# Kernel optimization log

Measured on AMD Instinct MI355X. Metric: run time of the kernel, lower is better.

The kernel has to match this reference:

```python
import jax, jax.numpy as jnp
import numpy as np

B, S, DIM = 1, 2048, 4096
NH, NKV, HD = 32, 8, 128
REPEATS = NH // NKV
ROPE_THETA = 10000.0


def setup_inputs() -> dict:
    key = jax.random.key(0)
    ks = jax.random.split(key, 6)
    x = jax.random.normal(ks[0], (B, S, DIM), jnp.float32) * 0.02
    wq = jax.random.normal(ks[1], (NH * HD, DIM), jnp.float32) * 0.02
    wk = jax.random.normal(ks[2], (NKV * HD, DIM), jnp.float32) * 0.02
    wv = jax.random.normal(ks[3], (NKV * HD, DIM), jnp.float32) * 0.02
    wo = jax.random.normal(ks[4], (DIM, NH * HD), jnp.float32) * 0.02
    # rotary frequencies (real cos/sin form of complex freqs_cis)
    inv_freq = 1.0 / (ROPE_THETA ** (jnp.arange(0, HD, 2, dtype=jnp.float32) / HD))
    ang = jnp.arange(S, dtype=jnp.float32)[:, None] * inv_freq[None, :]  # [S, HD//2]
    freqs_cos = jnp.cos(ang)
    freqs_sin = jnp.sin(ang)
    positions = jnp.arange(S, dtype=jnp.int32)  # prompt phase: all positions
    # additive causal mask
    mask = jnp.where(jnp.tril(jnp.ones((S, S), bool)), 0.0, -1e9).astype(jnp.float32)
    cache_k = jnp.zeros((B, S, NKV, HD), jnp.float32)
    cache_v = jnp.zeros((B, S, NKV, HD), jnp.float32)
    return dict(x=x, wq=wq, wk=wk, wv=wv, wo=wo, freqs_cos=freqs_cos,
                freqs_sin=freqs_sin, cache_k=cache_k, cache_v=cache_v,
                positions=positions, mask=mask)


def apply_rope(t, cos, sin):
    # t: [b, s, h, d]; pairs are (d0,d1),(d2,d3),... matching view_as_complex
    tr = t[..., 0::2]
    ti = t[..., 1::2]
    c = cos[None, :, None, :]
    s = sin[None, :, None, :]
    out_r = tr * c - ti * s
    out_i = tr * s + ti * c
    return jnp.stack([out_r, out_i], axis=-1).reshape(t.shape)


def reference(x, wq, wk, wv, wo, freqs_cos, freqs_sin, cache_k, cache_v, positions, mask):
    b, s, _ = x.shape
    xq = jnp.einsum('bsd,od->bso', x, wq).reshape(b, s, NH, HD)
    xk = jnp.einsum('bsd,od->bso', x, wk).reshape(b, s, NKV, HD)
    xv = jnp.einsum('bsd,od->bso', x, wv).reshape(b, s, NKV, HD)
    xq = apply_rope(xq, freqs_cos, freqs_sin)
    xk = apply_rope(xk, freqs_cos, freqs_sin)
    # KV-cache scatter (prompt phase writes; output uses fresh xk/xv here)
    cache_k = cache_k.at[:, positions].set(xk)
    cache_v = cache_v.at[:, positions].set(xv)
    # GQA: repeat_interleave kv heads to match query heads
    k = jnp.repeat(xk, REPEATS, axis=2).transpose(0, 2, 1, 3)  # [b, NH, s, HD]
    v = jnp.repeat(xv, REPEATS, axis=2).transpose(0, 2, 1, 3)
    q = xq.transpose(0, 2, 1, 3)
    scale = HD ** -0.5
    scores = jnp.einsum('bhqd,bhkd->bhqk', q, k) * scale + mask[None, None]
    probs = jax.nn.softmax(scores.astype(jnp.float32), axis=-1).astype(q.dtype)
    out = jnp.einsum('bhqk,bhkd->bhqd', probs, v)
    out = out.transpose(0, 2, 1, 3).reshape(b, s, NH * HD)
    return jnp.einsum('bso,do->bsd', out, wo)
```

## Files before the change

### kernel.cpp

```cpp
#include <hip/hip_runtime.h>
#include <hip/hip_bf16.h>
#include <stdint.h>

typedef __bf16 bf16_t;
typedef __attribute__((ext_vector_type(8))) __bf16 bf16x8;
typedef __attribute__((ext_vector_type(4))) float f32x4;
typedef __attribute__((ext_vector_type(8))) unsigned short u16x8;

#define S_LEN 2048
#define DIM   4096
#define QKVN  6144
#define NHEAD 32
#define HDIM  128

typedef __attribute__((address_space(1))) unsigned int as1_u32;
typedef __attribute__((address_space(3))) unsigned int as3_u32;

__device__ __forceinline__ unsigned short f2bf(float f) {
  unsigned u = __builtin_bit_cast(unsigned, f);
  u += 0x7fffu + ((u >> 16) & 1u);
  return (unsigned short)(u >> 16);
}

__device__ __forceinline__ void gload_lds16(const void* g, void* l) {
  __builtin_amdgcn_global_load_lds(
      (as1_u32*)(unsigned long long)(uintptr_t)g,
      (as3_u32*)(unsigned int)(uintptr_t)l,
      16, 0, 0);
}

__global__ __launch_bounds__(256) void cvt5_kernel(const float* __restrict__ x,
                                                   const float* __restrict__ wq,
                                                   const float* __restrict__ wk,
                                                   const float* __restrict__ wv,
                                                   const float* __restrict__ wo,
                                                   ushort4* __restrict__ xb,
                                                   ushort4* __restrict__ wqkvb,
                                                   ushort4* __restrict__ wob) {
  const long N0 = 2097152;
  const long N1 = N0 + 4194304;
  const long N2 = N1 + 1048576;
  const long N3 = N2 + 1048576;
  const long N4 = N3 + 4194304;
  long idx = (long)blockIdx.x * 256 + threadIdx.x;
  long stride = (long)gridDim.x * 256;
  for (long i = idx; i < N4; i += stride) {
    const float4* s; ushort4* d; long o;
    if (i < N0)      { s = (const float4*)x;  d = xb;              o = i; }
    else if (i < N1) { s = (const float4*)wq; d = wqkvb;           o = i - N0; }
    else if (i < N2) { s = (const float4*)wk; d = wqkvb + 4194304; o = i - N1; }
    else if (i < N3) { s = (const float4*)wv; d = wqkvb + 5242880; o = i - N2; }
    else             { s = (const float4*)wo; d = wob;             o = i - N3; }
    float4 v = s[o];
    ushort4 r;
    r.x = f2bf(v.x); r.y = f2bf(v.y); r.z = f2bf(v.z); r.w = f2bf(v.w);
    d[o] = r;
  }
}

__device__ __forceinline__ bf16x8 fld(const char* half, int row, int chunk) {
  return *(const bf16x8*)(half + row * 128 + ((chunk ^ (row & 7)) << 4));
}

template <int OUTF32>
__global__ __launch_bounds__(512, 2) void gemm8q(const bf16_t* __restrict__ A,
                                                 const bf16_t* __restrict__ B,
                                                 void* __restrict__ Cout,
                                                 int M, int N, int K, int nxt) {
  __shared__ char lds[114688];
  const int tid = threadIdx.x;
  const int lane = tid & 63, w = tid >> 6;
  const int wm = w >> 2, wn = w & 3;
  const int lg = lane >> 4, lr = lane & 15;
  const int nwg = gridDim.x;
  const int orig = blockIdx.x;
  const int wgid = (orig & 7) * (nwg >> 3) + (orig >> 3);
  const int bx = wgid % nxt, by = wgid / nxt;
  const long rowA = (long)by * 256;
  const long rowB = (long)bx * 192;

  f32x4 acc[8][3];
  const f32x4 z4 = {0.f, 0.f, 0.f, 0.f};
#pragma unroll
  for (int i = 0; i < 8; ++i)
#pragma unroll
    for (int j = 0; j < 3; ++j) acc[i][j] = z4;

  const int r0 = tid >> 3, sl = tid & 7;
  const long xo  = (long)((sl ^ (r0 & 7)) << 3);
  const long aof = (rowA + r0) * (long)K + xo;
  const long bof = (rowB + r0) * (long)K + xo;
  const long j1  = (long)64 * K;
  const long h1  = (long)128 * K;
  const int ld0 = tid * 16, ld1 = (tid + 512) * 16, ld2 = (tid + 1024) * 16;

#define QSTG_A(K0, HALF, DBUF)                                                 \
  { char* hp = lds + (DBUF) * 57344 + (HALF) * 16384;                          \
    gload_lds16(A + aof + (HALF) * h1 + (K0),      hp + ld0);                  \
    gload_lds16(A + aof + (HALF) * h1 + j1 + (K0), hp + ld1); }
#define QSTG_B(K0, DBUF)                                                       \
  { char* bp = lds + (DBUF) * 57344 + 32768;                                   \
    gload_lds16(B + bof + (K0),          bp + ld0);                            \
    gload_lds16(B + bof + j1 + (K0),     bp + ld1);                            \
    gload_lds16(B + bof + 2 * j1 + (K0), bp + ld2); }

  const int nt = K >> 6;
  const int brow = wn * 48;

  QSTG_A(0, 0, 0); QSTG_A(0, 1, 0); QSTG_B(0, 0);
  QSTG_B(64, 1);
  asm volatile("s_waitcnt vmcnt(3)" ::: "memory");
  __builtin_amdgcn_s_barrier();

  bf16x8 af[8][2], bf_[3][2];

  for (int t = 0; t < nt; ++t) {
    const int d = t & 1;
    const char* Ah = lds + d * 57344 + wm * 16384;
    const char* Br = lds + d * 57344 + 32768;
    const int k1 = (t + 1) << 6, k2 = (t + 2) << 6;
#pragma unroll
    for (int m = 0; m < 2; ++m) {
      af[m][0] = fld(Ah, m * 16 + lr, lg);
      af[m][1] = fld(Ah, m * 16 + lr, 4 + lg);
    }
#pragma unroll
    for (int n = 0; n < 3; ++n) {
      bf_[n][0] = fld(Br, brow + n * 16 + lr, lg);
      bf_[n][1] = fld(Br, brow + n * 16 + lr, 4 + lg);
    }
    if (t + 1 < nt) QSTG_A(k1, 0, d ^ 1);
    __builtin_amdgcn_s_barrier();
    asm volatile("s_waitcnt lgkmcnt(0)" ::: "memory");
    __builtin_amdgcn_sched_barrier(0);
    __builtin_amdgcn_s_setprio(1);
#pragma unroll
    for (int m = 0; m < 2; ++m)
#pragma unroll
      for (int n = 0; n < 3; ++n) {
        acc[m][n] = __builtin_amdgcn_mfma_f32_16x16x32_bf16(af[m][0], bf_[n][0], acc[m][n], 0, 0, 0);
        acc[m][n] = __builtin_amdgcn_mfma_f32_16x16x32_bf16(af[m][1], bf_[n][1], acc[m][n], 0, 0, 0);
      }
    __builtin_amdgcn_s_setprio(0);
    __builtin_amdgcn_s_barrier();
#pragma unroll
    for (int m = 2; m < 4; ++m) {
      af[m][0] = fld(Ah, m * 16 + lr, lg);
      af[m][1] = fld(Ah, m * 16 + lr, 4 + lg);
    }
    if (t + 1 < nt) QSTG_A(k1, 1, d ^ 1);
    __builtin_amdgcn_s_barrier();
    asm volatile("s_waitcnt lgkmcnt(0)" ::: "memory");
    __builtin_amdgcn_sched_barrier(0);
    __builtin_amdgcn_s_setprio(1);
#pragma unroll
    for (int m = 2; m < 4; ++m)
#pragma unroll
      for (int n = 0; n < 3; ++n) {
        acc[m][n] = __builtin_amdgcn_mfma_f32_16x16x32_bf16(af[m][0], bf_[n][0], acc[m][n], 0, 0, 0);
        acc[m][n] = __builtin_amdgcn_mfma_f32_16x16x32_bf16(af[m][1], bf_[n][1], acc[m][n], 0, 0, 0);
      }
    __builtin_amdgcn_s_setprio(0);
    __builtin_amdgcn_s_barrier();
#pragma unroll
    for (int m = 4; m < 6; ++m) {
      af[m][0] = fld(Ah, m * 16 + lr, lg);
      af[m][1] = fld(Ah, m * 16 + lr, 4 + lg);
    }
    if (t + 2 < nt) QSTG_B(k2, d);
    __builtin_amdgcn_s_barrier();
    asm volatile("s_waitcnt lgkmcnt(0)" ::: "memory");
    __builtin_amdgcn_sched_barrier(0);
    __builtin_amdgcn_s_setprio(1);
#pragma unroll
    for (int m = 4; m < 6; ++m)
#pragma unroll
      for (int n = 0; n < 3; ++n) {
        acc[m][n] = __builtin_amdgcn_mfma_f32_16x16x32_bf16(af[m][0], bf_[n][0], acc[m][n], 0, 0, 0);
        acc[m][n] = __builtin_amdgcn_mfma_f32_16x16x32_bf16(af[m][1], bf_[n][1], acc[m][n], 0, 0, 0);
      }
    __builtin_amdgcn_s_setprio(0);
    __builtin_amdgcn_s_barrier();
#pragma unroll
    for (int m = 6; m < 8; ++m) {
      af[m][0] = fld(Ah, m * 16 + lr, lg);
      af[m][1] = fld(Ah, m * 16 + lr, 4 + lg);
    }
    __builtin_amdgcn_s_barrier();
    asm volatile("s_waitcnt lgkmcnt(0)" ::: "memory");
    __builtin_amdgcn_sched_barrier(0);
    __builtin_amdgcn_s_setprio(1);
#pragma unroll
    for (int m = 6; m < 8; ++m)
#pragma unroll
      for (int n = 0; n < 3; ++n) {
        acc[m][n] = __builtin_amdgcn_mfma_f32_16x16x32_bf16(af[m][0], bf_[n][0], acc[m][n], 0, 0, 0);
        acc[m][n] = __builtin_amdgcn_mfma_f32_16x16x32_bf16(af[m][1], bf_[n][1], acc[m][n], 0, 0, 0);
      }
    __builtin_amdgcn_s_setprio(0);
    if (t + 2 < nt) {
      asm volatile("s_waitcnt vmcnt(3)" ::: "memory");
    } else {
      asm volatile("s_waitcnt vmcnt(0)" ::: "memory");
    }
    __builtin_amdgcn_s_barrier();
  }
#undef QSTG_A
#undef QSTG_B

  const long crow = rowA + wm * 128;
  const long ccol = rowB + wn * 48;
  if (OUTF32) {
    float* C = (float*)Cout;
#pragma unroll
    for (int mf = 0; mf < 8; ++mf)
#pragma unroll
      for (int j = 0; j < 4; ++j) {
        long row = crow + mf * 16 + lg * 4 + j;
        float* cp = C + row * N + ccol + lr;
#pragma unroll
        for (int nf = 0; nf < 3; ++nf) cp[nf * 16] = acc[mf][nf][j];
      }
  } else {
    unsigned short* C = (unsigned short*)Cout;
#pragma unroll
    for (int mf = 0; mf < 8; ++mf)
#pragma unroll
      for (int j = 0; j < 4; ++j) {
        long row = crow + mf * 16 + lg * 4 + j;
        unsigned short* cp = C + row * N + ccol + lr;
#pragma unroll
        for (int nf = 0; nf < 3; ++nf) cp[nf * 16] = f2bf(acc[mf][nf][j]);
      }
  }
}

template <int OUTF32>
__global__ __launch_bounds__(512, 2) void gemm8r(const bf16_t* __restrict__ A,
                                                 const bf16_t* __restrict__ B,
                                                 void* __restrict__ Cout,
                                                 int M, int N, int K, int nxt) {
  __shared__ char lds[98304];
  const int tid = threadIdx.x;
  const int lane = tid & 63, w = tid >> 6;
  const int wm = w >> 1, wn = w & 1;
  const int lg = lane >> 4, lr = lane & 15;
  const int nwg = gridDim.x;
  const int orig = blockIdx.x;
  const int wgid = (orig & 7) * (nwg >> 3) + (orig >> 3);
  const int bx = wgid % nxt, by = wgid / nxt;
  const long rowA = (long)by * 256;
  const long rowB = (long)bx * 128;

  f32x4 acc[4][4];
  const f32x4 z4 = {0.f, 0.f, 0.f, 0.f};
#pragma unroll
  for (int i = 0; i < 4; ++i)
#pragma unroll
    for (int j = 0; j < 4; ++j) acc[i][j] = z4;

  const int r0 = tid >> 3, sl = tid & 7;
  const long xo  = (long)((sl ^ (r0 & 7)) << 3);
  const long aof = (rowA + r0) * (long)K + xo;
  const long bof = (rowB + r0) * (long)K + xo;
  const long r64 = (long)64 * K;
  const int ld0 = tid * 16, ld1 = (tid + 512) * 16;

#define RSTG_A(K0, HALF, DBUF)                                                 \
  { char* ap = lds + (DBUF) * 49152 + (HALF) * 16384;                          \
    gload_lds16(A + aof + (HALF) * 2 * r64 + (K0),       ap + ld0);            \
    gload_lds16(A + aof + (HALF) * 2 * r64 + r64 + (K0), ap + ld1); }
#define RSTG_B(K0, DBUF)                                                       \
  { char* bp = lds + (DBUF) * 49152 + 32768;                                   \
    gload_lds16(B + bof + (K0),       bp + ld0);                               \
    gload_lds16(B + bof + r64 + (K0), bp + ld1); }

  const int nt = K >> 6;

  RSTG_A(0, 0, 0); RSTG_A(0, 1, 0); RSTG_B(0, 0);
  RSTG_B(64, 1);
  asm volatile("s_waitcnt vmcnt(2)" ::: "memory");
  __builtin_amdgcn_s_barrier();

  bf16x8 af[4][2], bf_[4][2];

  for (int t = 0; t < nt; ++t) {
    const int d = t & 1;
    const char* Ar = lds + d * 49152;
    const char* Br = Ar + 32768;
    const int arow = wm * 64, brow = wn * 64;
    const int k1 = (t + 1) << 6, k2 = (t + 2) << 6;
#pragma unroll
    for (int m = 0; m < 2; ++m) {
      af[m][0] = fld(Ar, arow + m * 16 + lr, lg);
      af[m][1] = fld(Ar, arow + m * 16 + lr, 4 + lg);
    }
#pragma unroll
    for (int n = 0; n < 2; ++n) {
      bf_[n][0] = fld(Br, brow + n * 16 + lr, lg);
      bf_[n][1] = fld(Br, brow + n * 16 + lr, 4 + lg);
    }
    if (t + 1 < nt) RSTG_A(k1, 0, d ^ 1);
    __builtin_amdgcn_s_barrier();
    asm volatile("s_waitcnt lgkmcnt(0)" ::: "memory");
    __builtin_amdgcn_sched_barrier(0);
    __builtin_amdgcn_s_setprio(1);
#pragma unroll
    for (int m = 0; m < 2; ++m)
#pragma unroll
      for (int n = 0; n < 2; ++n) {
        acc[m][n] = __builtin_amdgcn_mfma_f32_16x16x32_bf16(af[m][0], bf_[n][0], acc[m][n], 0, 0, 0);
        acc[m][n] = __builtin_amdgcn_mfma_f32_16x16x32_bf16(af[m][1], bf_[n][1], acc[m][n], 0, 0, 0);
      }
    __builtin_amdgcn_s_setprio(0);
    __builtin_amdgcn_s_barrier();
#pragma unroll
    for (int n = 2; n < 4; ++n) {
      bf_[n][0] = fld(Br, brow + n * 16 + lr, lg);
      bf_[n][1] = fld(Br, brow + n * 16 + lr, 4 + lg);
    }
    if (t + 1 < nt) RSTG_A(k1, 1, d ^ 1);
    __builtin_amdgcn_s_barrier();
    asm volatile("s_waitcnt lgkmcnt(0)" ::: "memory");
    __builtin_amdgcn_sched_barrier(0);
    __builtin_amdgcn_s_setprio(1);
#pragma unroll
    for (int m = 0; m < 2; ++m)
#pragma unroll
      for (int n = 2; n < 4; ++n) {
        acc[m][n] = __builtin_amdgcn_mfma_f32_16x16x32_bf16(af[m][0], bf_[n][0], acc[m][n], 0, 0, 0);
        acc[m][n] = __builtin_amdgcn_mfma_f32_16x16x32_bf16(af[m][1], bf_[n][1], acc[m][n], 0, 0, 0);
      }
    __builtin_amdgcn_s_setprio(0);
    __builtin_amdgcn_s_barrier();
#pragma unroll
    for (int m = 2; m < 4; ++m) {
      af[m][0] = fld(Ar, arow + m * 16 + lr, lg);
      af[m][1] = fld(Ar, arow + m * 16 + lr, 4 + lg);
    }
    if (t + 2 < nt) RSTG_B(k2, d);
    __builtin_amdgcn_s_barrier();
    asm volatile("s_waitcnt lgkmcnt(0)" ::: "memory");
    __builtin_amdgcn_sched_barrier(0);
    __builtin_amdgcn_s_setprio(1);
#pragma unroll
    for (int m = 2; m < 4; ++m)
#pragma unroll
      for (int n = 0; n < 2; ++n) {
        acc[m][n] = __builtin_amdgcn_mfma_f32_16x16x32_bf16(af[m][0], bf_[n][0], acc[m][n], 0, 0, 0);
        acc[m][n] = __builtin_amdgcn_mfma_f32_16x16x32_bf16(af[m][1], bf_[n][1], acc[m][n], 0, 0, 0);
      }
    __builtin_amdgcn_s_setprio(0);
    __builtin_amdgcn_s_barrier();
    __builtin_amdgcn_s_setprio(1);
#pragma unroll
    for (int m = 2; m < 4; ++m)
#pragma unroll
      for (int n = 2; n < 4; ++n) {
        acc[m][n] = __builtin_amdgcn_mfma_f32_16x16x32_bf16(af[m][0], bf_[n][0], acc[m][n], 0, 0, 0);
        acc[m][n] = __builtin_amdgcn_mfma_f32_16x16x32_bf16(af[m][1], bf_[n][1], acc[m][n], 0, 0, 0);
      }
    __builtin_amdgcn_s_setprio(0);
    if (t + 2 < nt) {
      asm volatile("s_waitcnt vmcnt(2)" ::: "memory");
    } else {
      asm volatile("s_waitcnt vmcnt(0)" ::: "memory");
    }
    __builtin_amdgcn_s_barrier();
  }
#undef RSTG_A
#undef RSTG_B

  const long crow = rowA + wm * 64;
  const long ccol = rowB + wn * 64;
  if (OUTF32) {
    float* C = (float*)Cout;
#pragma unroll
    for (int mf = 0; mf < 4; ++mf)
#pragma unroll
      for (int j = 0; j < 4; ++j) {
        long row = crow + mf * 16 + lg * 4 + j;
        float* cp = C + row * N + ccol + lr;
#pragma unroll
        for (int nf = 0; nf < 4; ++nf) cp[nf * 16] = acc[mf][nf][j];
      }
  } else {
    unsigned short* C = (unsigned short*)Cout;
#pragma unroll
    for (int mf = 0; mf < 4; ++mf)
#pragma unroll
      for (int j = 0; j < 4; ++j) {
        long row = crow + mf * 16 + lg * 4 + j;
        unsigned short* cp = C + row * N + ccol + lr;
#pragma unroll
        for (int nf = 0; nf < 4; ++nf) cp[nf * 16] = f2bf(acc[mf][nf][j]);
      }
  }
}

__global__ __launch_bounds__(256) void rope_kernel(unsigned int* __restrict__ qkv32,
                                                   const float* __restrict__ cosb,
                                                   const float* __restrict__ sinb) {
  int t = blockIdx.x * 256 + threadIdx.x;
  int i  = t & 63;
  int sh = t >> 6;
  int hh = sh % 40;
  int s  = sh / 40;
  int col2 = (hh < 32) ? (hh * 64 + i) : (2048 + (hh - 32) * 64 + i);
  unsigned int* p = qkv32 + (long)s * (QKVN / 2) + col2;
  unsigned int v = *p;
  float tr = __builtin_bit_cast(float, (v & 0xffffu) << 16);
  float ti = __builtin_bit_cast(float, v & 0xffff0000u);
  float c  = cosb[s * 64 + i];
  float sn = sinb[s * 64 + i];
  float orr = tr * c - ti * sn;
  float oi  = tr * sn + ti * c;
  *p = (unsigned int)f2bf(orr) | ((unsigned int)f2bf(oi) << 16);
}

__global__ __launch_bounds__(256) void vtrans_kernel(const bf16_t* __restrict__ qkv,
                                                     bf16_t* __restrict__ vT) {
  const int kh = blockIdx.x;
  const int hd = threadIdx.x & 127;
  const int s0 = blockIdx.y * 16 + (threadIdx.x >> 7) * 8;
  u16x8 v;
#pragma unroll
  for (int e = 0; e < 8; ++e)
    v[e] = *(const unsigned short*)(qkv + (long)(s0 + e) * QKVN + 5120 + kh * HDIM + hd);
  *(u16x8*)(vT + ((long)kh * HDIM + hd) * S_LEN + s0) = v;
}

__global__ __launch_bounds__(512) void attn_kernel(const bf16_t* __restrict__ qkv,
                                                   const bf16_t* __restrict__ vT,
                                                   unsigned short* __restrict__ ob) {
  __shared__ bf16_t Kt[64 * 128];
  __shared__ bf16_t Vt[128 * 64];
  __shared__ bf16_t Pl[8 * 16 * 64];
  const int h  = blockIdx.x;
  const int qi = 15 - (int)blockIdx.y;
  const int qb = qi * 128;
  const int kh = h >> 2;
  const int tid = threadIdx.x, lane = tid & 63, w = tid >> 6;
  const int lg = lane >> 4, lr = lane & 15;
  const int qrow0 = qb + w * 16;

  bf16x8 qf[4];
  const bf16_t* qptr = qkv + (long)(qrow0 + lr) * QKVN + h * HDIM + lg * 8;
#pragma unroll
  for (int kk = 0; kk < 4; ++kk) qf[kk] = *(const bf16x8*)(qptr + kk * 32);

  const f32x4 z4 = {0.f, 0.f, 0.f, 0.f};
  f32x4 oacc[8];
#pragma unroll
  for (int c = 0; c < 8; ++c) oacc[c] = z4;
  float m[4]    = {-1e30f, -1e30f, -1e30f, -1e30f};
  float lsum[4] = {0.f, 0.f, 0.f, 0.f};

  char* KtB = (char*)Kt;
  char* VtB = (char*)Vt;
  char* PlB = (char*)Pl + w * 2048;
  const float scale = 0.08838834764831845f;
  const int ntiles = 2 * qi + 2;
  const int wqmax = qrow0 + 15;

  for (int t = 0; t < ntiles; ++t) {
    const int kv0 = t * 64;
    __syncthreads();
#pragma unroll
    for (int it = 0; it < 2; ++it) {
      int cch = tid + it * 512;
      int r = cch >> 4, c = cch & 15;
      const bf16_t* src = qkv + (long)(kv0 + r) * QKVN + 4096 + kh * HDIM
                          + ((c ^ (r & 7)) * 8);
      gload_lds16(src, KtB + cch * 16);
    }
#pragma unroll
    for (int it = 0; it < 2; ++it) {
      int cch = tid + it * 512;
      int hd = cch >> 3, c = cch & 7;
      const bf16_t* src = vT + ((long)kh * HDIM + hd) * S_LEN + kv0
                          + ((c ^ (hd & 7)) * 8);
      gload_lds16(src, VtB + cch * 16);
    }
    __syncthreads();
    if (kv0 > wqmax) continue;

    f32x4 sf[4];
#pragma unroll
    for (int f = 0; f < 4; ++f) {
      f32x4 a = z4;
      int n = f * 16 + lr;
      int rb = n * 256, sw = (n & 7) << 4;
#pragma unroll
      for (int kk = 0; kk < 4; ++kk) {
        bf16x8 kf = *(const bf16x8*)(KtB + rb + (((kk * 4 + lg) * 16) ^ sw));
        a = __builtin_amdgcn_mfma_f32_16x16x32_bf16(qf[kk], kf, a, 0, 0, 0);
      }
      sf[f] = a;
    }

    float sc_arr[4];
#pragma unroll
    for (int j = 0; j < 4; ++j) {
      int qrow = qrow0 + lg * 4 + j;
      float sv[4];
#pragma unroll
      for (int f = 0; f < 4; ++f) {
        float s = sf[f][j] * scale;
        if (kv0 + f * 16 + lr > qrow) s = -1e9f;
        sv[f] = s;
      }
      float mx = fmaxf(fmaxf(sv[0], sv[1]), fmaxf(sv[2], sv[3]));
      mx = fmaxf(mx, __shfl_xor(mx, 1));
      mx = fmaxf(mx, __shfl_xor(mx, 2));
      mx = fmaxf(mx, __shfl_xor(mx, 4));
      mx = fmaxf(mx, __shfl_xor(mx, 8));
      float mn = fmaxf(m[j], mx);
      float p[4];
#pragma unroll
      for (int f = 0; f < 4; ++f) p[f] = __expf(sv[f] - mn);
      float ps = (p[0] + p[1]) + (p[2] + p[3]);
      ps += __shfl_xor(ps, 1);
      ps += __shfl_xor(ps, 2);
      ps += __shfl_xor(ps, 4);
      ps += __shfl_xor(ps, 8);
      float sc = __expf(m[j] - mn);
      lsum[j] = lsum[j] * sc + ps;
      m[j] = mn;
      sc_arr[j] = sc;
      int row = lg * 4 + j;
      int swp = (row & 7) << 4;
#pragma unroll
      for (int f = 0; f < 4; ++f)
        *(unsigned short*)(PlB + row * 128 + (((f * 16 + lr) * 2) ^ swp)) = f2bf(p[f]);
    }
#pragma unroll
    for (int c = 0; c < 8; ++c)
#pragma unroll
      for (int j = 0; j < 4; ++j) oacc[c][j] *= sc_arr[j];

    bf16x8 pfr[2];
#pragma unroll
    for (int kk = 0; kk < 2; ++kk)
      pfr[kk] = *(const bf16x8*)(PlB + lr * 128 + (((kk * 4 + lg) * 16) ^ ((lr & 7) << 4)));
#pragma unroll
    for (int c = 0; c < 8; ++c) {
      int hd = c * 16 + lr;
      int rb = hd * 128, sw = (hd & 7) << 4;
#pragma unroll
      for (int kk = 0; kk < 2; ++kk) {
        bf16x8 vf = *(const bf16x8*)(VtB + rb + (((kk * 4 + lg) * 16) ^ sw));
        oacc[c] = __builtin_amdgcn_mfma_f32_16x16x32_bf16(pfr[kk], vf, oacc[c], 0, 0, 0);
      }
    }
  }

  float rl[4];
#pragma unroll
  for (int j = 0; j < 4; ++j) rl[j] = 1.f / lsum[j];
#pragma unroll
  for (int c = 0; c < 8; ++c)
#pragma unroll
    for (int j = 0; j < 4; ++j) {
      long row = qrow0 + lg * 4 + j;
      ob[row * 4096 + h * 128 + c * 16 + lr] = f2bf(oacc[c][j] * rl[j]);
    }
}

extern "C" void kernel_launch(void* const* d_in, const int* in_sizes, int n_in,
                              void* d_out, int out_size, void* d_ws, size_t ws_size,
                              hipStream_t stream) {
  const float* x  = (const float*)d_in[0];
  const float* wq = (const float*)d_in[1];
  const float* wk = (const float*)d_in[2];
  const float* wv = (const float*)d_in[3];
  const float* wo = (const float*)d_in[4];
  const float* fc = (const float*)d_in[5];
  const float* fs = (const float*)d_in[6];

  char* ws = (char*)d_ws;
  bf16_t* xb    = (bf16_t*)(ws + 0);
  bf16_t* wqkvb = (bf16_t*)(ws + 16777216);
  bf16_t* wob   = (bf16_t*)(ws + 67108864);
  bf16_t* qkv   = (bf16_t*)(ws + 100663296);
  bf16_t* ob    = (bf16_t*)(ws + 125829120);
  bf16_t* vT    = (bf16_t*)(ws + 0);

  cvt5_kernel<<<2048, 256, 0, stream>>>(x, wq, wk, wv, wo,
                                        (ushort4*)xb, (ushort4*)wqkvb, (ushort4*)wob);

  gemm8q<0><<<256, 512, 0, stream>>>(xb, wqkvb, qkv, 2048, 6144, 4096, 32);
  vtrans_kernel<<<dim3(8, 128), 256, 0, stream>>>(qkv, vT);
  rope_kernel<<<20480, 256, 0, stream>>>((unsigned int*)qkv, fc, fs);
  attn_kernel<<<dim3(32, 16), 512, 0, stream>>>(qkv, vT, (unsigned short*)ob);
  gemm8r<1><<<256, 512, 0, stream>>>(ob, wob, d_out, 2048, 4096, 4096, 32);
}
```

Measured before the change: 324.4 us.

## Triple-buffer output GEMM, simplify QKV epilogue, streamline attention softmax rescaling

The output-projection GEMM moves from double to triple buffering, using 144KB of LDS. It prefetches two K-tiles ahead and needs fewer barrier phases per iteration. The attention softmax now works in base-2 with a raw v_exp_f32, skips causal masking on fully unmasked tiles, and rescales the accumulators only when some row max grows. The QKV GEMM epilogue loses its unused f32 branch. The 144KB LDS request at 2 blocks per CU may lower occupancy or exceed the LDS limit.

Result: no change. 320.9 us (-1.1%).

```diff
diff --git a/kernel.cpp b/kernel.cpp
--- a/kernel.cpp
+++ b/kernel.cpp
@@ -210,37 +210,24 @@
 
   const long crow = rowA + wm * 128;
   const long ccol = rowB + wn * 48;
-  if (OUTF32) {
-    float* C = (float*)Cout;
-#pragma unroll
-    for (int mf = 0; mf < 8; ++mf)
-#pragma unroll
-      for (int j = 0; j < 4; ++j) {
-        long row = crow + mf * 16 + lg * 4 + j;
-        float* cp = C + row * N + ccol + lr;
-#pragma unroll
-        for (int nf = 0; nf < 3; ++nf) cp[nf * 16] = acc[mf][nf][j];
-      }
-  } else {
-    unsigned short* C = (unsigned short*)Cout;
-#pragma unroll
-    for (int mf = 0; mf < 8; ++mf)
-#pragma unroll
-      for (int j = 0; j < 4; ++j) {
-        long row = crow + mf * 16 + lg * 4 + j;
-        unsigned short* cp = C + row * N + ccol + lr;
-#pragma unroll
-        for (int nf = 0; nf < 3; ++nf) cp[nf * 16] = f2bf(acc[mf][nf][j]);
-      }
-  }
+  unsigned short* C = (unsigned short*)Cout;
+#pragma unroll
+  for (int mf = 0; mf < 8; ++mf)
+#pragma unroll
+    for (int j = 0; j < 4; ++j) {
+      long row = crow + mf * 16 + lg * 4 + j;
+      unsigned short* cp = C + row * N + ccol + lr;
+#pragma unroll
+      for (int nf = 0; nf < 3; ++nf) cp[nf * 16] = f2bf(acc[mf][nf][j]);
+    }
 }
 
 template <int OUTF32>
-__global__ __launch_bounds__(512, 2) void gemm8r(const bf16_t* __restrict__ A,
+__global__ __launch_bounds__(512, 2) void gemm2p(const bf16_t* __restrict__ A,
                                                  const bf16_t* __restrict__ B,
                                                  void* __restrict__ Cout,
                                                  int M, int N, int K, int nxt) {
-  __shared__ char lds[98304];
+  __shared__ char lds[147456];
   const int tid = threadIdx.x;
   const int lane = tid & 63, w = tid >> 6;
   const int wm = w >> 1, wn = w & 1;
@@ -264,49 +251,49 @@
   const long aof = (rowA + r0) * (long)K + xo;
   const long bof = (rowB + r0) * (long)K + xo;
   const long r64 = (long)64 * K;
-  const int ld0 = tid * 16, ld1 = (tid + 512) * 16;
-
-#define RSTG_A(K0, HALF, DBUF)                                                 \
-  { char* ap = lds + (DBUF) * 49152 + (HALF) * 16384;                          \
-    gload_lds16(A + aof + (HALF) * 2 * r64 + (K0),       ap + ld0);            \
-    gload_lds16(A + aof + (HALF) * 2 * r64 + r64 + (K0), ap + ld1); }
-#define RSTG_B(K0, DBUF)                                                       \
-  { char* bp = lds + (DBUF) * 49152 + 32768;                                   \
-    gload_lds16(B + bof + (K0),       bp + ld0);                               \
-    gload_lds16(B + bof + r64 + (K0), bp + ld1); }
+
+#define PSTG_A(K0, BUF)                                                        \
+  { char* ap = lds + (BUF) * 32768;                                            \
+    gload_lds16(A + aof + (K0),           ap + tid * 16);                      \
+    gload_lds16(A + aof + r64 + (K0),     ap + (tid + 512) * 16);              \
+    gload_lds16(A + aof + 2 * r64 + (K0), ap + (tid + 1024) * 16);             \
+    gload_lds16(A + aof + 3 * r64 + (K0), ap + (tid + 1536) * 16); }
+#define PSTG_B(K0, BUF)                                                        \
+  { char* bp = lds + 98304 + (BUF) * 16384;                                    \
+    gload_lds16(B + bof + (K0),       bp + tid * 16);                          \
+    gload_lds16(B + bof + r64 + (K0), bp + (tid + 512) * 16); }
 
   const int nt = K >> 6;
 
-  RSTG_A(0, 0, 0); RSTG_A(0, 1, 0); RSTG_B(0, 0);
-  RSTG_B(64, 1);
-  asm volatile("s_waitcnt vmcnt(2)" ::: "memory");
+  PSTG_A(0, 0); PSTG_B(0, 0); PSTG_A(64, 1); PSTG_B(64, 1);
+  asm volatile("s_waitcnt vmcnt(6)" ::: "memory");
   __builtin_amdgcn_s_barrier();
 
   bf16x8 af[4][2], bf_[4][2];
 
   for (int t = 0; t < nt; ++t) {
-    const int d = t & 1;
-    const char* Ar = lds + d * 49152;
-    const char* Br = Ar + 32768;
+    const int b3 = t % 3, s3 = (t + 2) % 3;
+    const char* Ab = lds + b3 * 32768;
+    const char* Bb = lds + 98304 + b3 * 16384;
     const int arow = wm * 64, brow = wn * 64;
-    const int k1 = (t + 1) << 6, k2 = (t + 2) << 6;
-#pragma unroll
-    for (int m = 0; m < 2; ++m) {
-      af[m][0] = fld(Ar, arow + m * 16 + lr, lg);
-      af[m][1] = fld(Ar, arow + m * 16 + lr, 4 + lg);
+    const int k2 = (t + 2) << 6;
+#pragma unroll
+    for (int m = 0; m < 4; ++m) {
+      af[m][0] = fld(Ab, arow + m * 16 + lr, lg);
+      af[m][1] = fld(Ab, arow + m * 16 + lr, 4 + lg);
     }
 #pragma unroll
     for (int n = 0; n < 2; ++n) {
-      bf_[n][0] = fld(Br, brow + n * 16 + lr, lg);
-      bf_[n][1] = fld(Br, brow + n * 16 + lr, 4 + lg);
-    }
-    if (t + 1 < nt) RSTG_A(k1, 0, d ^ 1);
+      bf_[n][0] = fld(Bb, brow + n * 16 + lr, lg);
+      bf_[n][1] = fld(Bb, brow + n * 16 + lr, 4 + lg);
+    }
+    if (t + 2 < nt) PSTG_A(k2, s3);
     __builtin_amdgcn_s_barrier();
     asm volatile("s_waitcnt lgkmcnt(0)" ::: "memory");
     __builtin_amdgcn_sched_barrier(0);
     __builtin_amdgcn_s_setprio(1);
 #pragma unroll
-    for (int m = 0; m < 2; ++m)
+    for (int m = 0; m < 4; ++m)
 #pragma unroll
       for (int n = 0; n < 2; ++n) {
         acc[m][n] = __builtin_amdgcn_mfma_f32_16x16x32_bf16(af[m][0], bf_[n][0], acc[m][n], 0, 0, 0);
@@ -316,60 +303,31 @@
     __builtin_amdgcn_s_barrier();
 #pragma unroll
     for (int n = 2; n < 4; ++n) {
-      bf_[n][0] = fld(Br, brow + n * 16 + lr, lg);
-      bf_[n][1] = fld(Br, brow + n * 16 + lr, 4 + lg);
-    }
-    if (t + 1 < nt) RSTG_A(k1, 1, d ^ 1);
+      bf_[n][0] = fld(Bb, brow + n * 16 + lr, lg);
+      bf_[n][1] = fld(Bb, brow + n * 16 + lr, 4 + lg);
+    }
+    if (t + 2 < nt) PSTG_B(k2, s3);
     __builtin_amdgcn_s_barrier();
     asm volatile("s_waitcnt lgkmcnt(0)" ::: "memory");
     __builtin_amdgcn_sched_barrier(0);
     __builtin_amdgcn_s_setprio(1);
 #pragma unroll
-    for (int m = 0; m < 2; ++m)
+    for (int m = 0; m < 4; ++m)
 #pragma unroll
       for (int n = 2; n < 4; ++n) {
         acc[m][n] = __builtin_amdgcn_mfma_f32_16x16x32_bf16(af[m][0], bf_[n][0], acc[m][n], 0, 0, 0);
         acc[m][n] = __builtin_amdgcn_mfma_f32_16x16x32_bf16(af[m][1], bf_[n][1], acc[m][n], 0, 0, 0);
       }
     __builtin_amdgcn_s_setprio(0);
-    __builtin_amdgcn_s_barrier();
-#pragma unroll
-    for (int m = 2; m < 4; ++m) {
-      af[m][0] = fld(Ar, arow + m * 16 + lr, lg);
-      af[m][1] = fld(Ar, arow + m * 16 + lr, 4 + lg);
-    }
-    if (t + 2 < nt) RSTG_B(k2, d);
-    __builtin_amdgcn_s_barrier();
-    asm volatile("s_waitcnt lgkmcnt(0)" ::: "memory");
-    __builtin_amdgcn_sched_barrier(0);
-    __builtin_amdgcn_s_setprio(1);
-#pragma unroll
-    for (int m = 2; m < 4; ++m)
-#pragma unroll
-      for (int n = 0; n < 2; ++n) {
-        acc[m][n] = __builtin_amdgcn_mfma_f32_16x16x32_bf16(af[m][0], bf_[n][0], acc[m][n], 0, 0, 0);
-        acc[m][n] = __builtin_amdgcn_mfma_f32_16x16x32_bf16(af[m][1], bf_[n][1], acc[m][n], 0, 0, 0);
-      }
-    __builtin_amdgcn_s_setprio(0);
-    __builtin_amdgcn_s_barrier();
-    __builtin_amdgcn_s_setprio(1);
-#pragma unroll
-    for (int m = 2; m < 4; ++m)
-#pragma unroll
-      for (int n = 2; n < 4; ++n) {
-        acc[m][n] = __builtin_amdgcn_mfma_f32_16x16x32_bf16(af[m][0], bf_[n][0], acc[m][n], 0, 0, 0);
-        acc[m][n] = __builtin_amdgcn_mfma_f32_16x16x32_bf16(af[m][1], bf_[n][1], acc[m][n], 0, 0, 0);
-      }
-    __builtin_amdgcn_s_setprio(0);
     if (t + 2 < nt) {
-      asm volatile("s_waitcnt vmcnt(2)" ::: "memory");
+      asm volatile("s_waitcnt vmcnt(6)" ::: "memory");
     } else {
       asm volatile("s_waitcnt vmcnt(0)" ::: "memory");
     }
     __builtin_amdgcn_s_barrier();
   }
-#undef RSTG_A
-#undef RSTG_B
+#undef PSTG_A
+#undef PSTG_B
 
   const long crow = rowA + wm * 64;
   const long ccol = rowB + wn * 64;
@@ -459,7 +417,7 @@
   char* KtB = (char*)Kt;
   char* VtB = (char*)Vt;
   char* PlB = (char*)Pl + w * 2048;
-  const float scale = 0.08838834764831845f;
+  const float SCL2 = 0.08838834764831845f * 1.44269504088896f;
   const int ntiles = 2 * qi + 2;
   const int wqmax = qrow0 + 15;
 
@@ -499,45 +457,69 @@
       sf[f] = a;
     }
 
-    float sc_arr[4];
+    float sv[4][4], mx[4];
+    if (kv0 + 63 <= qrow0) {
+#pragma unroll
+      for (int j = 0; j < 4; ++j) {
+#pragma unroll
+        for (int f = 0; f < 4; ++f) sv[j][f] = sf[f][j] * SCL2;
+        float t0 = fmaxf(fmaxf(sv[j][0], sv[j][1]), fmaxf(sv[j][2], sv[j][3]));
+        t0 = fmaxf(t0, __shfl_xor(t0, 1));
+        t0 = fmaxf(t0, __shfl_xor(t0, 2));
+        t0 = fmaxf(t0, __shfl_xor(t0, 4));
+        t0 = fmaxf(t0, __shfl_xor(t0, 8));
+        mx[j] = t0;
+      }
+    } else {
+#pragma unroll
+      for (int j = 0; j < 4; ++j) {
+        int qrow = qrow0 + lg * 4 + j;
+#pragma unroll
+        for (int f = 0; f < 4; ++f) {
+          float s = sf[f][j] * SCL2;
+          if (kv0 + f * 16 + lr > qrow) s = -1e9f;
+          sv[j][f] = s;
+        }
+        float t0 = fmaxf(fmaxf(sv[j][0], sv[j][1]), fmaxf(sv[j][2], sv[j][3]));
+        t0 = fmaxf(t0, __shfl_xor(t0, 1));
+        t0 = fmaxf(t0, __shfl_xor(t0, 2));
+        t0 = fmaxf(t0, __shfl_xor(t0, 4));
+        t0 = fmaxf(t0, __shfl_xor(t0, 8));
+        mx[j] = t0;
+      }
+    }
+    float g = fmaxf(fmaxf(mx[0] - m[0], mx[1] - m[1]),
+                    fmaxf(mx[2] - m[2], mx[3] - m[3]));
+    if (__any(g > 0.f)) {
+#pragma unroll
+      for (int j = 0; j < 4; ++j) {
+        float mn = fmaxf(m[j], mx[j]);
+        float sc;
+        asm("v_exp_f32 %0, %1" : "=v"(sc) : "v"(m[j] - mn));
+        lsum[j] *= sc;
+        m[j] = mn;
+#pragma unroll
+        for (int c = 0; c < 8; ++c) oacc[c][j] *= sc;
+      }
+    }
 #pragma unroll
     for (int j = 0; j < 4; ++j) {
-      int qrow = qrow0 + lg * 4 + j;
-      float sv[4];
-#pragma unroll
-      for (int f = 0; f < 4; ++f) {
-        float s = sf[f][j] * scale;
-        if (kv0 + f * 16 + lr > qrow) s = -1e9f;
-        sv[f] = s;
-      }
-      float mx = fmaxf(fmaxf(sv[0], sv[1]), fmaxf(sv[2], sv[3]));
-      mx = fmaxf(mx, __shfl_xor(mx, 1));
-      mx = fmaxf(mx, __shfl_xor(mx, 2));
-      mx = fmaxf(mx, __shfl_xor(mx, 4));
-      mx = fmaxf(mx, __shfl_xor(mx, 8));
-      float mn = fmaxf(m[j], mx);
       float p[4];
 #pragma unroll
-      for (int f = 0; f < 4; ++f) p[f] = __expf(sv[f] - mn);
+      for (int f = 0; f < 4; ++f)
+        asm("v_exp_f32 %0, %1" : "=v"(p[f]) : "v"(sv[j][f] - m[j]));
       float ps = (p[0] + p[1]) + (p[2] + p[3]);
       ps += __shfl_xor(ps, 1);
       ps += __shfl_xor(ps, 2);
       ps += __shfl_xor(ps, 4);
       ps += __shfl_xor(ps, 8);
-      float sc = __expf(m[j] - mn);
-      lsum[j] = lsum[j] * sc + ps;
-      m[j] = mn;
-      sc_arr[j] = sc;
+      lsum[j] += ps;
       int row = lg * 4 + j;
       int swp = (row & 7) << 4;
 #pragma unroll
       for (int f = 0; f < 4; ++f)
         *(unsigned short*)(PlB + row * 128 + (((f * 16 + lr) * 2) ^ swp)) = f2bf(p[f]);
     }
-#pragma unroll
-    for (int c = 0; c < 8; ++c)
-#pragma unroll
-      for (int j = 0; j < 4; ++j) oacc[c][j] *= sc_arr[j];
 
     bf16x8 pfr[2];
 #pragma unroll
@@ -593,5 +575,5 @@
   vtrans_kernel<<<dim3(8, 128), 256, 0, stream>>>(qkv, vT);
   rope_kernel<<<20480, 256, 0, stream>>>((unsigned int*)qkv, fc, fs);
   attn_kernel<<<dim3(32, 16), 512, 0, stream>>>(qkv, vT, (unsigned short*)ob);
-  gemm8r<1><<<256, 512, 0, stream>>>(ob, wob, d_out, 2048, 4096, 4096, 32);
-}
+  gemm2p<1><<<256, 512, 0, stream>>>(ob, wob, d_out, 2048, 4096, 4096, 32);
+}
```
